# Kernel optimization log

Hardware: AMD Instinct MI355X
Metric: run time of the kernel (lower is better)

## Reference

```python
import jax, jax.numpy as jnp
from jax import lax
import numpy as np

NUM_EMBEDDINGS = 8192
EMBEDDING_DIM = 256
COMMITMENT_COST = 0.25


def setup_inputs() -> dict:
    key = jax.random.key(0)
    k1, k2 = jax.random.split(key)
    z = jax.random.normal(k1, (16, EMBEDDING_DIM, 32, 32), dtype=jnp.float32)
    codebook = jax.random.uniform(
        k2, (NUM_EMBEDDINGS, EMBEDDING_DIM), dtype=jnp.float32,
        minval=-1.0 / NUM_EMBEDDINGS, maxval=1.0 / NUM_EMBEDDINGS)
    return {"z": z, "codebook": codebook}


def reference(z, codebook):
    B, C, H, W = z.shape  # C == embedding_dim
    zp = jnp.transpose(z, (0, 2, 3, 1))          # [B, H, W, C]
    z_flat = zp.reshape(-1, C)                    # [N, C], N = B*H*W
    # squared-distance via ||z||^2 + ||e||^2 - 2 z.e
    z2 = jnp.sum(z_flat * z_flat, axis=1, keepdims=True)   # [N, 1]
    e2 = jnp.sum(codebook * codebook, axis=1)               # [K]
    ez = z_flat @ codebook.T                                # [N, K]
    distances = z2 + e2 - 2.0 * ez                          # [N, K]
    e_indices = jnp.argmin(distances, axis=1)               # [N]
    z_q = codebook[e_indices]                               # [N, C]
    # Faithfully reproduce the original's mislabeled unpack:
    # torch does B, D, H, W = z.shape on the BHWC tensor, then
    # z_q.view(B, H, W, D).permute(0, 3, 1, 2) == reshape(B, W, C, H) -> (0,3,1,2)
    z_q = jnp.transpose(z_q.reshape(B, W, C, H), (0, 3, 1, 2))  # [B, H, W, C]
    commitment_loss = jnp.mean((lax.stop_gradient(zp) - z_q) ** 2)
    codebook_loss = jnp.mean((zp - lax.stop_gradient(z_q)) ** 2)
    loss = codebook_loss + COMMITMENT_COST * commitment_loss
    z_q_st = zp + lax.stop_gradient(z_q - zp)   # straight-through, [B, H, W, C]
    return z_q_st, loss, e_indices
```

## Files before the change

### kernel.cpp

```cpp
#include <hip/hip_runtime.h>
#include <stdint.h>

#define NROWS 16384
#define KENT  8192
#define CDIM  256
#define NELEM 4194304

#define ZSCALE 22.0f
#define ESCALE 1040384.0f
#define MARGIN_INT 4096
#define SBIAS 4194304


typedef int v4i __attribute__((ext_vector_type(4)));

__device__ inline int q8(float x, float s) {
    int v = __float2int_rn(x * s);
    return v < -127 ? -127 : (v > 127 ? 127 : v);
}
__device__ inline unsigned pk4(int a, int b, int c, int d) {
    return (a & 255) | ((b & 255) << 8) | ((c & 255) << 16) | ((d & 255) << 24);
}
__device__ inline unsigned umax_(unsigned a, unsigned b) { return a > b ? a : b; }
__device__ inline unsigned umin_(unsigned a, unsigned b) { return a < b ? a : b; }
__device__ inline void gload_lds16(const void* g, void* l) {
    __builtin_amdgcn_global_load_lds(
        (const __attribute__((address_space(1))) void*)g,
        (__attribute__((address_space(3))) void*)l, 16, 0, 0);
}

__global__ __launch_bounds__(256) void vq_prep(
        const float* __restrict__ z, const float* __restrict__ cb,
        float* __restrict__ z2w, char* __restrict__ zbi8,
        char* __restrict__ cbbi8, float* __restrict__ loss_out) {
    const int t = threadIdx.x;
    const int bid = blockIdx.x;

    if (bid >= 256) {
        const int ppi = bid - 256;
        const int p = ppi >> 1, h = ppi & 1;
        const int r = t & 63, qh = t >> 6;
        const int row = h * 64 + r;
        char* dst = cbbi8 + p * 32768;
        const float* src = cb + (p * 128 + row) * 256;
#pragma unroll
        for (int qq = 0; qq < 4; ++qq) {
            const int q = qh * 4 + qq;
            float4 a = *(const float4*)(src + q * 16);
            float4 b = *(const float4*)(src + q * 16 + 4);
            float4 c = *(const float4*)(src + q * 16 + 8);
            float4 d = *(const float4*)(src + q * 16 + 12);
            uint4 v;
            v.x = pk4(q8(a.x,ESCALE), q8(a.y,ESCALE), q8(a.z,ESCALE), q8(a.w,ESCALE));
            v.y = pk4(q8(b.x,ESCALE), q8(b.y,ESCALE), q8(b.z,ESCALE), q8(b.w,ESCALE));
            v.z = pk4(q8(c.x,ESCALE), q8(c.y,ESCALE), q8(c.z,ESCALE), q8(c.w,ESCALE));
            v.w = pk4(q8(d.x,ESCALE), q8(d.y,ESCALE), q8(d.z,ESCALE), q8(d.w,ESCALE));
            *(uint4*)&dst[(q * 128 + row) * 16] = v;
        }
        if (ppi == 0 && t == 0) loss_out[0] = 0.f;
        return;
    }

    __shared__ float pprt[2][64][17];
    __shared__ float s64[64];
    const int r = t & 63;
    const int part = t >> 6;
    const int blk = part >> 1, jh = part & 1;
    const int n = bid * 64 + r;
    const int b = n >> 10, hw = n & 1023;
    const float* base = z + b * 262144 + hw;

    const int p = n >> 7, rp = n & 127;
    char* dst = zbi8 + p * 32768;

    float t0[16], p01[16], pr[16];

#pragma unroll
    for (int jj = 0; jj < 4; ++jj) {
        const int j = jh * 4 + jj;
        float a[16];
#pragma unroll
        for (int L = 0; L < 16; ++L)
            a[L] = base[(blk * 128 + L + 16 * j) * 1024];
        int qb[16];
#pragma unroll
        for (int L = 0; L < 16; ++L) {
            qb[L] = q8(a[L], ZSCALE);
            float sq = a[L] * a[L];
            asm volatile("" : "+v"(sq));
            if (jj == 0)      t0[L] = sq;
            else if (jj == 1) p01[L] = t0[L] + sq;
            else if (jj == 2) t0[L] = sq;
            else              pr[L] = p01[L] + (t0[L] + sq);
        }
        uint4 v;
        v.x = pk4(qb[0], qb[1], qb[2], qb[3]);
        v.y = pk4(qb[4], qb[5], qb[6], qb[7]);
        v.z = pk4(qb[8], qb[9], qb[10], qb[11]);
        v.w = pk4(qb[12], qb[13], qb[14], qb[15]);
        *(uint4*)&dst[((blk * 8 + j) * 128 + rp) * 16] = v;
    }

    if (jh == 1) {
#pragma unroll
        for (int L = 0; L < 16; ++L) pprt[blk][r][L] = pr[L];
    }
    __syncthreads();
    float bs = 0.f;
    if (jh == 0) {
        float C[16];
#pragma unroll
        for (int L = 0; L < 16; ++L) C[L] = pr[L] + pprt[blk][r][L];
        float t8[8];
#pragma unroll
        for (int L = 0; L < 8; ++L) t8[L] = C[L] + C[L + 8];
        float t4[4];
#pragma unroll
        for (int L = 0; L < 4; ++L) t4[L] = t8[L] + t8[L + 4];
        float t2a = t4[0] + t4[2];
        float t2b = t4[1] + t4[3];
        bs = t2a + t2b;
        if (blk == 1) s64[r] = bs;
    }
    __syncthreads();
    if (part == 0) z2w[n] = bs + s64[r];
}

__global__ __launch_bounds__(256, 4) void vq_gemm(
        const char* __restrict__ zbi8,
        const char* __restrict__ cbbi8,
        unsigned long long* __restrict__ gstats) {
    __shared__ __align__(16) char smem[32768];

    const int tid = threadIdx.x;
    const int w = tid >> 6, l = tid & 63;
    const int q4 = l >> 4, cl = l & 15;
    const int mw = w & 1, nw = w >> 1;

    const unsigned bx = blockIdx.x;
    const unsigned xcd = bx & 7, local = bx >> 3;
    const unsigned png = local >> 8;
    const unsigned rem = local & 255;
    const unsigned pm = (rem >> 4) * 8 + xcd;
    const unsigned pn = png * 16 + (rem & 15);

    const char* Ab = zbi8 + pm * 32768;
    const char* Bb = cbbi8 + pn * 32768;

#pragma unroll
    for (int u = 0; u < 8; ++u)
        gload_lds16(Ab + u * 4096 + tid * 16, smem + u * 4096 + (w << 10));

    const char* abase = Bb + (q4 * 128 + mw * 64 + cl) * 16;
    v4i af[4], afn[4];
#pragma unroll
    for (int i = 0; i < 4; ++i)
        af[i] = *(const v4i*)(abase + i * 256);

    const unsigned vb = ((unsigned)SBIAS << 6) + (unsigned)(q4 * 4);

    v4i acc[4][4];
    __syncthreads();

#pragma unroll
    for (int kt = 0; kt < 4; ++kt) {
        v4i bfl[4];
#pragma unroll
        for (int j = 0; j < 4; ++j)
            bfl[j] = *(const v4i*)(smem + kt * 8192 + q4 * 2048
                                        + nw * 1024 + j * 256 + cl * 16);
        if (kt < 3) {
#pragma unroll
            for (int i = 0; i < 4; ++i)
                afn[i] = *(const v4i*)(abase + (kt + 1) * 8192 + i * 256);
        }
        __builtin_amdgcn_s_setprio(1);
#pragma unroll
        for (int i = 0; i < 4; ++i)
#pragma unroll
            for (int j = 0; j < 4; ++j) {
                if (kt == 0)
                    acc[i][j] = __builtin_amdgcn_mfma_i32_16x16x64_i8(
                        af[i], bfl[j], (v4i)0, 0, 0, 0);
                else
                    acc[i][j] = __builtin_amdgcn_mfma_i32_16x16x64_i8(
                        af[i], bfl[j], acc[i][j], 0, 0, 0);
            }
        __builtin_amdgcn_s_setprio(0);
#pragma unroll
        for (int i = 0; i < 4; ++i) af[i] = afn[i];
    }

    unsigned long long* gs = gstats + (pn * 2 + (unsigned)mw) * 16384u
                                    + pm * 128u + (unsigned)(nw * 64);
#pragma unroll
    for (int jj = 0; jj < 4; ++jj) {
        unsigned m1[8], m2[8];
#pragma unroll
        for (int i = 0; i < 4; ++i)
#pragma unroll
            for (int gp = 0; gp < 2; ++gp) {
                unsigned pa = ((unsigned)acc[i][jj][2 * gp] << 6)
                              + vb + (unsigned)(i * 16 + 2 * gp);
                unsigned pb = ((unsigned)acc[i][jj][2 * gp + 1] << 6)
                              + vb + (unsigned)(i * 16 + 2 * gp + 1);
                m1[i * 2 + gp] = umax_(pa, pb);
                m2[i * 2 + gp] = umin_(pa, pb);
            }
#pragma unroll
        for (int s = 4; s >= 1; s >>= 1)
#pragma unroll
            for (int u = 0; u < 4; ++u) {
                if (u < s) {
                    unsigned a1 = m1[u], a2 = m2[u];
                    unsigned b1 = m1[u + s], b2 = m2[u + s];
                    m1[u] = umax_(a1, b1);
                    m2[u] = umax_(umin_(a1, b1), umax_(a2, b2));
                }
            }
        unsigned t1 = m1[0], t2 = m2[0];
#pragma unroll
        for (int off = 16; off <= 32; off <<= 1) {
            unsigned o1 = (unsigned)__shfl_xor((int)t1, off);
            unsigned o2 = (unsigned)__shfl_xor((int)t2, off);
            t2 = umax_(umax_(t2, o2), umin_(t1, o1));
            t1 = umax_(t1, o1);
        }
        if (q4 == 0)
            gs[jj * 16 + cl] =
                ((unsigned long long)t1 << 32) | (unsigned long long)t2;
    }
}

__global__ __launch_bounds__(256) void vq_finalize(
        const float* __restrict__ z, const float* __restrict__ cb,
        const float* __restrict__ z2w,
        const unsigned long long* __restrict__ gstats,
        float* __restrict__ out, float* __restrict__ out_idx) {
    __shared__ float zs[32][32];
    __shared__ unsigned pmax[8][32];
    __shared__ int thrL[32];
    __shared__ unsigned candL[512];
    __shared__ unsigned blkcnt;
    __shared__ unsigned long long bestL[32];
    __shared__ float tile[32 * 257];

    const int t = threadIdx.x;
    const int bid = blockIdx.x;
    const int n0 = bid * 32;
    const int b = bid >> 5, j = bid & 31;
    const int hw0 = j * 32;
    const int r = t & 31, gc = t >> 5;

    unsigned long long e[16];
    unsigned m = 0;
#pragma unroll
    for (int g2 = 0; g2 < 16; ++g2) {
        e[g2] = gstats[(size_t)(gc * 16 + g2) * 16384u + (unsigned)(n0 + r)];
        m = umax_(m, (unsigned)(e[g2] >> 32));
    }
    pmax[gc][r] = m;
    if (t == 0) blkcnt = 0;
    __syncthreads();
    if (t < 32) {
        unsigned mm = 0;
#pragma unroll
        for (int g = 0; g < 8; ++g) mm = umax_(mm, pmax[g][t]);
        thrL[t] = (int)(mm >> 6) - MARGIN_INT;
        bestL[t] = ~0ull;
    }
    __syncthreads();

    {
        int th = thrL[r];
#pragma unroll
        for (int g2 = 0; g2 < 16; ++g2) {
            unsigned p1 = (unsigned)(e[g2] >> 32), p2 = (unsigned)e[g2];
            unsigned kb = (unsigned)(gc * 16 + g2) * 64u;
            if ((int)(p1 >> 6) >= th) {
                unsigned pos = atomicAdd(&blkcnt, 1u);
                if (pos < 512u)
                    candL[pos] = ((unsigned)r << 13) | (kb + (p1 & 63u));
            }
            if ((int)(p2 >> 6) >= th) {
                unsigned pos = atomicAdd(&blkcnt, 1u);
                if (pos < 512u)
                    candL[pos] = ((unsigned)r << 13) | (kb + (p2 & 63u));
            }
        }
    }
    __syncthreads();
    int ns = (int)(blkcnt < 512u ? blkcnt : 512u);

    for (int base = 0; base < ns; base += 256) {
        bool active = base + t < ns;
        int rr0 = 0, k = 0;
        if (active) {
            unsigned v = candL[base + t];
            rr0 = v >> 13; k = v & 8191;
        }
        float sacc = 0.f;
        for (int ch = 0; ch < 8; ++ch) {
            __syncthreads();
            {
                int rr = t & 31, cc2 = t >> 5;
#pragma unroll
                for (int u = 0; u < 4; ++u) {
                    int cc = u * 8 + cc2;
                    zs[cc][rr] = z[b * 262144 + (ch * 32 + cc) * 1024 + hw0 + rr];
                }
            }
            __syncthreads();
            if (active) {
                const float4* cbp = (const float4*)(cb + k * 256 + ch * 32);
                float4 A0 = cbp[0], A1 = cbp[1], A2 = cbp[2], A3 = cbp[3];
                float4 A4 = cbp[4], A5 = cbp[5], A6 = cbp[6], A7 = cbp[7];
                float Af[32] = {A0.x,A0.y,A0.z,A0.w, A1.x,A1.y,A1.z,A1.w,
                                A2.x,A2.y,A2.z,A2.w, A3.x,A3.y,A3.z,A3.w,
                                A4.x,A4.y,A4.z,A4.w, A5.x,A5.y,A5.z,A5.w,
                                A6.x,A6.y,A6.z,A6.w, A7.x,A7.y,A7.z,A7.w};
#pragma unroll
                for (int u = 0; u < 32; ++u)
                    sacc = __builtin_fmaf(zs[u][rr0], Af[u], sacc);
            }
        }
        if (active) {
            float d = z2w[n0 + rr0] - 2.0f * sacc;
            unsigned long long key =
                ((unsigned long long)__float_as_uint(d) << 32) | (unsigned)k;
            atomicMin(&bestL[rr0], key);
        }
    }
    __syncthreads();
    if (t < 32)
        out_idx[n0 + t] = (float)(unsigned)(bestL[t] & 0xFFFFFFFFu);

    {
        const int c0 = t & 63;
        const int w0 = (t >> 6) * 8;
#pragma unroll
        for (int it = 0; it < 8; ++it) {
            int wr = w0 + it;
            int kk = (int)(unsigned)(bestL[wr] & 0xFFFFFFFFu);
            const float* src = cb + kk * 256 + c0;
            float* drow = tile + wr * 257 + c0;
            drow[0]   = src[0];
            drow[64]  = src[64];
            drow[128] = src[128];
            drow[192] = src[192];
        }
    }
    __syncthreads();

    float* obase = out + b * 262144 + j * 256;
    const int wv = t >> 3, cb8 = (t & 7) * 32;
#pragma unroll
    for (int it = 0; it < 32; ++it)
        obase[it * 8192 + t] = tile[wv * 257 + cb8 + it];
}

__global__ __launch_bounds__(256) void vq_loss(
        const float* __restrict__ z, const float* __restrict__ out,
        float* __restrict__ loss_out) {
    __shared__ float zs[256][33];
    __shared__ float wsum[4];

    const int t = threadIdx.x;
    const int b = blockIdx.x >> 5, i = blockIdx.x & 31;

#pragma unroll
    for (int it = 0; it < 32; ++it) {
        int k = it * 8 + (t >> 5);
        zs[k][t & 31] = z[b * 262144 + k * 1024 + i * 32 + (t & 31)];
    }
    __syncthreads();

    const float* ob = out + b * 262144 + i * 8192;
    float lsum = 0.f;
#pragma unroll 4
    for (int it = 0; it < 32; ++it) {
        float d = zs[t][it] - ob[it * 256 + t];
        lsum = __builtin_fmaf(d, d, lsum);
    }
#pragma unroll
    for (int off = 32; off >= 1; off >>= 1) lsum += __shfl_down(lsum, off, 64);
    int lane = t & 63, wv = t >> 6;
    if (lane == 0) wsum[wv] = lsum;
    __syncthreads();
    if (t == 0)
        atomicAdd(loss_out, (wsum[0] + wsum[1] + wsum[2] + wsum[3]) *
                            (1.25f / (float)NELEM));
}

extern "C" void kernel_launch(void* const* d_in, const int* in_sizes, int n_in,
                              void* d_out, int out_size, void* d_ws, size_t ws_size,
                              hipStream_t stream) {
    const float* z  = (const float*)d_in[0];
    const float* cb = (const float*)d_in[1];
    float* out = (float*)d_out;

    char* ws = (char*)d_ws;
    char* zbi8               = ws;
    char* cbbi8              = ws + 4194304;
    unsigned long long* gstats = (unsigned long long*)(ws + 6291456);
    float* z2w               = (float*)(ws + 23068672);

    vq_prep<<<384, 256, 0, stream>>>(z, cb, z2w, zbi8, cbbi8, out + NELEM);

    vq_gemm<<<8192, 256, 0, stream>>>(zbi8, cbbi8, gstats);

    vq_finalize<<<512, 256, 0, stream>>>(z, cb, z2w, gstats,
                                         out, out + NELEM + 1);

    vq_loss<<<512, 256, 0, stream>>>(z, out, out + NELEM);
}
```

Baseline: 147.3 us.

## Make GEMM blocks persistent over codebook tiles and stage full z tile in finalize

The int8 distance GEMM now launches 1024 blocks instead of 8192. Each block loads a z tile into LDS once and loops over 4 codebook tiles for each of 2 row tiles, which removes repeated LDS staging and block launch overhead. In the finalize kernel, the whole 256x32 z slice is loaded into shared memory up front instead of in 8 chunks with two barriers each, so candidate rescoring runs without syncthreads. The risks are less parallelism and less latency hiding in the GEMM, and a larger shared footprint in finalize (about 32KB more), which may lower occupancy.

```diff
diff --git a/kernel.cpp b/kernel.cpp
--- a/kernel.cpp
+++ b/kernel.cpp
@@ -137,98 +137,104 @@
     const int q4 = l >> 4, cl = l & 15;
     const int mw = w & 1, nw = w >> 1;
 
-    const unsigned bx = blockIdx.x;
-    const unsigned xcd = bx & 7, local = bx >> 3;
-    const unsigned png = local >> 8;
-    const unsigned rem = local & 255;
-    const unsigned pm = (rem >> 4) * 8 + xcd;
-    const unsigned pn = png * 16 + (rem & 15);
-
-    const char* Ab = zbi8 + pm * 32768;
-    const char* Bb = cbbi8 + pn * 32768;
-
-#pragma unroll
-    for (int u = 0; u < 8; ++u)
-        gload_lds16(Ab + u * 4096 + tid * 16, smem + u * 4096 + (w << 10));
-
-    const char* abase = Bb + (q4 * 128 + mw * 64 + cl) * 16;
-    v4i af[4], afn[4];
-#pragma unroll
-    for (int i = 0; i < 4; ++i)
-        af[i] = *(const v4i*)(abase + i * 256);
-
+    const unsigned xcd = (unsigned)blockIdx.x & 7u;
+    const unsigned local0 = (unsigned)blockIdx.x >> 3;
     const unsigned vb = ((unsigned)SBIAS << 6) + (unsigned)(q4 * 4);
 
-    v4i acc[4][4];
-    __syncthreads();
-
-#pragma unroll
-    for (int kt = 0; kt < 4; ++kt) {
-        v4i bfl[4];
-#pragma unroll
-        for (int j = 0; j < 4; ++j)
-            bfl[j] = *(const v4i*)(smem + kt * 8192 + q4 * 2048
-                                        + nw * 1024 + j * 256 + cl * 16);
-        if (kt < 3) {
+#pragma unroll 1
+    for (int ph = 0; ph < 2; ++ph) {
+        const unsigned rem = (local0 + (unsigned)ph * 128u) & 255u;
+        const unsigned pm = (rem >> 4) * 8u + xcd;
+        const char* Ab = zbi8 + pm * 32768u;
+
+        __syncthreads();
+#pragma unroll
+        for (int u = 0; u < 8; ++u)
+            gload_lds16(Ab + u * 4096 + tid * 16, smem + u * 4096 + (w << 10));
+
+#pragma unroll 1
+        for (int png = 0; png < 4; ++png) {
+            const unsigned pn = (unsigned)png * 16u + (rem & 15u);
+            const char* abase = cbbi8 + pn * 32768u
+                              + (q4 * 128 + mw * 64 + cl) * 16;
+            v4i af[4], afn[4];
 #pragma unroll
             for (int i = 0; i < 4; ++i)
-                afn[i] = *(const v4i*)(abase + (kt + 1) * 8192 + i * 256);
-        }
-        __builtin_amdgcn_s_setprio(1);
-#pragma unroll
-        for (int i = 0; i < 4; ++i)
-#pragma unroll
-            for (int j = 0; j < 4; ++j) {
-                if (kt == 0)
-                    acc[i][j] = __builtin_amdgcn_mfma_i32_16x16x64_i8(
-                        af[i], bfl[j], (v4i)0, 0, 0, 0);
-                else
-                    acc[i][j] = __builtin_amdgcn_mfma_i32_16x16x64_i8(
-                        af[i], bfl[j], acc[i][j], 0, 0, 0);
+                af[i] = *(const v4i*)(abase + i * 256);
+
+            v4i acc[4][4];
+            if (png == 0) __syncthreads();
+
+#pragma unroll
+            for (int kt = 0; kt < 4; ++kt) {
+                v4i bfl[4];
+#pragma unroll
+                for (int j = 0; j < 4; ++j)
+                    bfl[j] = *(const v4i*)(smem + kt * 8192 + q4 * 2048
+                                           + nw * 1024 + j * 256 + cl * 16);
+                if (kt < 3) {
+#pragma unroll
+                    for (int i = 0; i < 4; ++i)
+                        afn[i] = *(const v4i*)(abase + (kt + 1) * 8192 + i * 256);
+                }
+                __builtin_amdgcn_s_setprio(1);
+#pragma unroll
+                for (int i = 0; i < 4; ++i)
+#pragma unroll
+                    for (int j = 0; j < 4; ++j) {
+                        if (kt == 0)
+                            acc[i][j] = __builtin_amdgcn_mfma_i32_16x16x64_i8(
+                                af[i], bfl[j], (v4i)0, 0, 0, 0);
+                        else
+                            acc[i][j] = __builtin_amdgcn_mfma_i32_16x16x64_i8(
+                                af[i], bfl[j], acc[i][j], 0, 0, 0);
+                    }
+                __builtin_amdgcn_s_setprio(0);
+#pragma unroll
+                for (int i = 0; i < 4; ++i) af[i] = afn[i];
             }
-        __builtin_amdgcn_s_setprio(0);
-#pragma unroll
-        for (int i = 0; i < 4; ++i) af[i] = afn[i];
-    }
-
-    unsigned long long* gs = gstats + (pn * 2 + (unsigned)mw) * 16384u
-                                    + pm * 128u + (unsigned)(nw * 64);
-#pragma unroll
-    for (int jj = 0; jj < 4; ++jj) {
-        unsigned m1[8], m2[8];
-#pragma unroll
-        for (int i = 0; i < 4; ++i)
-#pragma unroll
-            for (int gp = 0; gp < 2; ++gp) {
-                unsigned pa = ((unsigned)acc[i][jj][2 * gp] << 6)
-                              + vb + (unsigned)(i * 16 + 2 * gp);
-                unsigned pb = ((unsigned)acc[i][jj][2 * gp + 1] << 6)
-                              + vb + (unsigned)(i * 16 + 2 * gp + 1);
-                m1[i * 2 + gp] = umax_(pa, pb);
-                m2[i * 2 + gp] = umin_(pa, pb);
+
+            unsigned long long* gs = gstats
+                + (pn * 2 + (unsigned)mw) * 16384u
+                + pm * 128u + (unsigned)(nw * 64);
+#pragma unroll
+            for (int jj = 0; jj < 4; ++jj) {
+                unsigned m1[8], m2[8];
+#pragma unroll
+                for (int i = 0; i < 4; ++i)
+#pragma unroll
+                    for (int gp = 0; gp < 2; ++gp) {
+                        unsigned pa = ((unsigned)acc[i][jj][2 * gp] << 6)
+                                      + vb + (unsigned)(i * 16 + 2 * gp);
+                        unsigned pb = ((unsigned)acc[i][jj][2 * gp + 1] << 6)
+                                      + vb + (unsigned)(i * 16 + 2 * gp + 1);
+                        m1[i * 2 + gp] = umax_(pa, pb);
+                        m2[i * 2 + gp] = umin_(pa, pb);
+                    }
+#pragma unroll
+                for (int s = 4; s >= 1; s >>= 1)
+#pragma unroll
+                    for (int u = 0; u < 4; ++u) {
+                        if (u < s) {
+                            unsigned a1 = m1[u], a2 = m2[u];
+                            unsigned b1 = m1[u + s], b2 = m2[u + s];
+                            m1[u] = umax_(a1, b1);
+                            m2[u] = umax_(umin_(a1, b1), umax_(a2, b2));
+                        }
+                    }
+                unsigned t1 = m1[0], t2 = m2[0];
+#pragma unroll
+                for (int off = 16; off <= 32; off <<= 1) {
+                    unsigned o1 = (unsigned)__shfl_xor((int)t1, off);
+                    unsigned o2 = (unsigned)__shfl_xor((int)t2, off);
+                    t2 = umax_(umax_(t2, o2), umin_(t1, o1));
+                    t1 = umax_(t1, o1);
+                }
+                if (q4 == 0)
+                    gs[jj * 16 + cl] =
+                        ((unsigned long long)t1 << 32) | (unsigned long long)t2;
             }
-#pragma unroll
-        for (int s = 4; s >= 1; s >>= 1)
-#pragma unroll
-            for (int u = 0; u < 4; ++u) {
-                if (u < s) {
-                    unsigned a1 = m1[u], a2 = m2[u];
-                    unsigned b1 = m1[u + s], b2 = m2[u + s];
-                    m1[u] = umax_(a1, b1);
-                    m2[u] = umax_(umin_(a1, b1), umax_(a2, b2));
-                }
-            }
-        unsigned t1 = m1[0], t2 = m2[0];
-#pragma unroll
-        for (int off = 16; off <= 32; off <<= 1) {
-            unsigned o1 = (unsigned)__shfl_xor((int)t1, off);
-            unsigned o2 = (unsigned)__shfl_xor((int)t2, off);
-            t2 = umax_(umax_(t2, o2), umin_(t1, o1));
-            t1 = umax_(t1, o1);
-        }
-        if (q4 == 0)
-            gs[jj * 16 + cl] =
-                ((unsigned long long)t1 << 32) | (unsigned long long)t2;
+        }
     }
 }
 
@@ -237,7 +243,7 @@
         const float* __restrict__ z2w,
         const unsigned long long* __restrict__ gstats,
         float* __restrict__ out, float* __restrict__ out_idx) {
-    __shared__ float zs[32][32];
+    __shared__ float zs[256][32];
     __shared__ unsigned pmax[8][32];
     __shared__ int thrL[32];
     __shared__ unsigned candL[512];
@@ -251,6 +257,15 @@
     const int b = bid >> 5, j = bid & 31;
     const int hw0 = j * 32;
     const int r = t & 31, gc = t >> 5;
+
+    {
+        const int rr = t & 31, cc2 = t >> 5;
+#pragma unroll
+        for (int u = 0; u < 32; ++u) {
+            int cc = u * 8 + cc2;
+            zs[cc][rr] = z[b * 262144 + cc * 1024 + hw0 + rr];
+        }
+    }
 
     unsigned long long e[16];
     unsigned m = 0;
@@ -293,25 +308,12 @@
     int ns = (int)(blkcnt < 512u ? blkcnt : 512u);
 
     for (int base = 0; base < ns; base += 256) {
-        bool active = base + t < ns;
-        int rr0 = 0, k = 0;
-        if (active) {
+        if (base + t < ns) {
             unsigned v = candL[base + t];
-            rr0 = v >> 13; k = v & 8191;
-        }
-        float sacc = 0.f;
-        for (int ch = 0; ch < 8; ++ch) {
-            __syncthreads();
-            {
-                int rr = t & 31, cc2 = t >> 5;
-#pragma unroll
-                for (int u = 0; u < 4; ++u) {
-                    int cc = u * 8 + cc2;
-                    zs[cc][rr] = z[b * 262144 + (ch * 32 + cc) * 1024 + hw0 + rr];
-                }
-            }
-            __syncthreads();
-            if (active) {
+            int rr0 = v >> 13, k = v & 8191;
+            float sacc = 0.f;
+#pragma unroll 1
+            for (int ch = 0; ch < 8; ++ch) {
                 const float4* cbp = (const float4*)(cb + k * 256 + ch * 32);
                 float4 A0 = cbp[0], A1 = cbp[1], A2 = cbp[2], A3 = cbp[3];
                 float4 A4 = cbp[4], A5 = cbp[5], A6 = cbp[6], A7 = cbp[7];
@@ -321,10 +323,8 @@
                                 A6.x,A6.y,A6.z,A6.w, A7.x,A7.y,A7.z,A7.w};
 #pragma unroll
                 for (int u = 0; u < 32; ++u)
-                    sacc = __builtin_fmaf(zs[u][rr0], Af[u], sacc);
+                    sacc = __builtin_fmaf(zs[ch * 32 + u][rr0], Af[u], sacc);
             }
-        }
-        if (active) {
             float d = z2w[n0 + rr0] - 2.0f * sacc;
             unsigned long long key =
                 ((unsigned long long)__float_as_uint(d) << 32) | (unsigned)k;
@@ -407,7 +407,7 @@
 
     vq_prep<<<384, 256, 0, stream>>>(z, cb, z2w, zbi8, cbbi8, out + NELEM);
 
-    vq_gemm<<<8192, 256, 0, stream>>>(zbi8, cbbi8, gstats);
+    vq_gemm<<<1024, 256, 0, stream>>>(zbi8, cbbi8, gstats);
 
     vq_finalize<<<512, 256, 0, stream>>>(z, cb, z2w, gstats,
                                          out, out + NELEM + 1);
```

New measurement: 143.8 us. 1.02x faster.

## Stage full z tile in LDS, fold bias into MFMA init, use permlane swaps

Applied to the files above, without the earlier changes.

The finalize kernel now loads the whole 256x32 z tile into shared memory once at the start. This removes the per-chunk reload and the two barriers per chunk inside the candidate rescoring loop, so candidate threads run without block-wide syncs. In the GEMM kernel, the SBIAS offset is folded into the accumulator initial value of the first MFMA instead of being added in the epilogue. The cross-lane top-2 reduction now uses v_permlane16/32_swap instead of __shfl_xor. The larger 32KB LDS array may reduce occupancy of the finalize kernel.

```diff
diff --git a/kernel.cpp b/kernel.cpp
--- a/kernel.cpp
+++ b/kernel.cpp
@@ -157,7 +157,8 @@
     for (int i = 0; i < 4; ++i)
         af[i] = *(const v4i*)(abase + i * 256);
 
-    const unsigned vb = ((unsigned)SBIAS << 6) + (unsigned)(q4 * 4);
+    const unsigned colb = (unsigned)(q4 * 4);
+    const v4i cinit = (v4i)SBIAS;
 
     v4i acc[4][4];
     __syncthreads();
@@ -181,7 +182,7 @@
             for (int j = 0; j < 4; ++j) {
                 if (kt == 0)
                     acc[i][j] = __builtin_amdgcn_mfma_i32_16x16x64_i8(
-                        af[i], bfl[j], (v4i)0, 0, 0, 0);
+                        af[i], bfl[j], cinit, 0, 0, 0);
                 else
                     acc[i][j] = __builtin_amdgcn_mfma_i32_16x16x64_i8(
                         af[i], bfl[j], acc[i][j], 0, 0, 0);
@@ -201,9 +202,9 @@
 #pragma unroll
             for (int gp = 0; gp < 2; ++gp) {
                 unsigned pa = ((unsigned)acc[i][jj][2 * gp] << 6)
-                              + vb + (unsigned)(i * 16 + 2 * gp);
+                              + (colb + (unsigned)(i * 16 + 2 * gp));
                 unsigned pb = ((unsigned)acc[i][jj][2 * gp + 1] << 6)
-                              + vb + (unsigned)(i * 16 + 2 * gp + 1);
+                              + (colb + (unsigned)(i * 16 + 2 * gp + 1));
                 m1[i * 2 + gp] = umax_(pa, pb);
                 m2[i * 2 + gp] = umin_(pa, pb);
             }
@@ -219,12 +220,19 @@
                 }
             }
         unsigned t1 = m1[0], t2 = m2[0];
-#pragma unroll
-        for (int off = 16; off <= 32; off <<= 1) {
-            unsigned o1 = (unsigned)__shfl_xor((int)t1, off);
-            unsigned o2 = (unsigned)__shfl_xor((int)t2, off);
-            t2 = umax_(umax_(t2, o2), umin_(t1, o1));
-            t1 = umax_(t1, o1);
+        {
+            unsigned a1 = t1, b1 = t1, a2 = t2, b2 = t2;
+            asm volatile("v_permlane16_swap_b32 %0, %1" : "+v"(a1), "+v"(b1));
+            asm volatile("v_permlane16_swap_b32 %0, %1" : "+v"(a2), "+v"(b2));
+            t2 = umax_(umin_(a1, b1), umax_(a2, b2));
+            t1 = umax_(a1, b1);
+        }
+        {
+            unsigned a1 = t1, b1 = t1, a2 = t2, b2 = t2;
+            asm volatile("v_permlane32_swap_b32 %0, %1" : "+v"(a1), "+v"(b1));
+            asm volatile("v_permlane32_swap_b32 %0, %1" : "+v"(a2), "+v"(b2));
+            t2 = umax_(umin_(a1, b1), umax_(a2, b2));
+            t1 = umax_(a1, b1);
         }
         if (q4 == 0)
             gs[jj * 16 + cl] =
@@ -237,7 +245,7 @@
         const float* __restrict__ z2w,
         const unsigned long long* __restrict__ gstats,
         float* __restrict__ out, float* __restrict__ out_idx) {
-    __shared__ float zs[32][32];
+    __shared__ float zs[256][32];
     __shared__ unsigned pmax[8][32];
     __shared__ int thrL[32];
     __shared__ unsigned candL[512];
@@ -251,6 +259,15 @@
     const int b = bid >> 5, j = bid & 31;
     const int hw0 = j * 32;
     const int r = t & 31, gc = t >> 5;
+
+    {
+        const int rr = t & 31, cc2 = t >> 5;
+#pragma unroll
+        for (int u = 0; u < 32; ++u) {
+            int cc = u * 8 + cc2;
+            zs[cc][rr] = z[b * 262144 + cc * 1024 + hw0 + rr];
+        }
+    }
 
     unsigned long long e[16];
     unsigned m = 0;
@@ -293,25 +310,12 @@
     int ns = (int)(blkcnt < 512u ? blkcnt : 512u);
 
     for (int base = 0; base < ns; base += 256) {
-        bool active = base + t < ns;
-        int rr0 = 0, k = 0;
-        if (active) {
+        if (base + t < ns) {
             unsigned v = candL[base + t];
-            rr0 = v >> 13; k = v & 8191;
-        }
-        float sacc = 0.f;
-        for (int ch = 0; ch < 8; ++ch) {
-            __syncthreads();
-            {
-                int rr = t & 31, cc2 = t >> 5;
-#pragma unroll
-                for (int u = 0; u < 4; ++u) {
-                    int cc = u * 8 + cc2;
-                    zs[cc][rr] = z[b * 262144 + (ch * 32 + cc) * 1024 + hw0 + rr];
-                }
-            }
-            __syncthreads();
-            if (active) {
+            int rr0 = v >> 13, k = v & 8191;
+            float sacc = 0.f;
+#pragma unroll 1
+            for (int ch = 0; ch < 8; ++ch) {
                 const float4* cbp = (const float4*)(cb + k * 256 + ch * 32);
                 float4 A0 = cbp[0], A1 = cbp[1], A2 = cbp[2], A3 = cbp[3];
                 float4 A4 = cbp[4], A5 = cbp[5], A6 = cbp[6], A7 = cbp[7];
@@ -321,10 +325,8 @@
                                 A6.x,A6.y,A6.z,A6.w, A7.x,A7.y,A7.z,A7.w};
 #pragma unroll
                 for (int u = 0; u < 32; ++u)
-                    sacc = __builtin_fmaf(zs[u][rr0], Af[u], sacc);
-            }
-        }
-        if (active) {
+                    sacc = __builtin_fmaf(zs[ch * 32 + u][rr0], Af[u], sacc);
+            }
             float d = z2w[n0 + rr0] - 2.0f * sacc;
             unsigned long long key =
                 ((unsigned long long)__float_as_uint(d) << 32) | (unsigned)k;
```

Result: no change. 149.4 us (+1.4%).
